# Optimization experiments

Hardware: AMD Instinct MI355X
Metric: run time of the kernel (lower is better)

The kernel has to match this reference:

```python
import jax, jax.numpy as jnp
import numpy as np

BN_EPS = 1e-5
N_NODES, N_EDGES, D_IN, HID = 100000, 1600000, 64, 128


def _bn(x, g, b, m, v):
    # BatchNorm1d in eval mode: running stats
    return (x - m) * jax.lax.rsqrt(v + BN_EPS) * g + b


def _gin_agg(x, edge_index, eps):
    # PyG GINConv aggregation: out[dst] = (1+eps)*x[dst] + sum_{src->dst} x[src]
    src, dst = edge_index[0], edge_index[1]
    s = jax.ops.segment_sum(x[src], dst, num_segments=x.shape[0])
    return (1.0 + eps) * x + s


def setup_inputs() -> dict:
    key = jax.random.key(0)
    ks = jax.random.split(key, 24)
    sc = 0.05
    d = {
        'x': jax.random.normal(ks[0], (N_NODES, D_IN), dtype=jnp.float32),
        'edge_index': jax.random.randint(ks[1], (2, N_EDGES), 0, N_NODES, dtype=jnp.int64),
        'eps1': jnp.zeros((), jnp.float32),
        'W1a': jax.random.normal(ks[2], (D_IN, HID), jnp.float32) * sc,
        'b1a': jnp.zeros((HID,), jnp.float32),
        'W1b': jax.random.normal(ks[3], (HID, HID), jnp.float32) * sc,
        'b1b': jnp.zeros((HID,), jnp.float32),
        'g1': jnp.ones((HID,), jnp.float32), 'be1': jnp.zeros((HID,), jnp.float32),
        'm1': jnp.zeros((HID,), jnp.float32), 'v1': jnp.ones((HID,), jnp.float32),
        'eps2': jnp.zeros((), jnp.float32),
        'W2a': jax.random.normal(ks[4], (HID, HID), jnp.float32) * sc,
        'b2a': jnp.zeros((HID,), jnp.float32),
        'g2': jnp.ones((HID,), jnp.float32), 'be2': jnp.zeros((HID,), jnp.float32),
        'm2': jnp.zeros((HID,), jnp.float32), 'v2': jnp.ones((HID,), jnp.float32),
        'eps3': jnp.zeros((), jnp.float32),
        'W3a': jax.random.normal(ks[5], (HID, HID), jnp.float32) * sc,
        'b3a': jnp.zeros((HID,), jnp.float32),
        'W3b': jax.random.normal(ks[6], (HID, HID), jnp.float32) * sc,
        'b3b': jnp.zeros((HID,), jnp.float32),
        'g3': jnp.ones((HID,), jnp.float32), 'be3': jnp.zeros((HID,), jnp.float32),
        'm3': jnp.zeros((HID,), jnp.float32), 'v3': jnp.ones((HID,), jnp.float32),
        'Wl': jax.random.normal(ks[7], (HID, HID), jnp.float32) * sc,
        'bl': jnp.zeros((HID,), jnp.float32),
        'Wf': jax.random.normal(ks[8], (HID, 1), jnp.float32) * sc,
        'bf': jnp.zeros((1,), jnp.float32),
    }
    return d


def reference(x, edge_index, eps1, W1a, b1a, W1b, b1b, g1, be1, m1, v1,
              eps2, W2a, b2a, g2, be2, m2, v2,
              eps3, W3a, b3a, W3b, b3b, g3, be3, m3, v3,
              Wl, bl, Wf, bf):
    # GINConv 1: agg -> Linear(64,128) ReLU -> Linear(128,128) ReLU -> BN
    h = _gin_agg(x, edge_index, eps1)
    h = jax.nn.relu(h @ W1a + b1a)
    h = jax.nn.relu(h @ W1b + b1b)
    h = _bn(h, g1, be1, m1, v1)
    # GINConv 2: agg -> Linear ReLU -> BN
    h = _gin_agg(h, edge_index, eps2)
    h = jax.nn.relu(h @ W2a + b2a)
    h = _bn(h, g2, be2, m2, v2)
    # GINConv 3: agg -> Linear ReLU -> Linear ReLU -> BN
    h = _gin_agg(h, edge_index, eps3)
    h = jax.nn.relu(h @ W3a + b3a)
    h = jax.nn.relu(h @ W3b + b3b)
    h = _bn(h, g3, be3, m3, v3)
    # head: lin1 + ReLU (dropout identity in eval), fc, squeeze
    h = jax.nn.relu(h @ Wl + bl)
    out = (h @ Wf + bf).squeeze(-1)  # [N]
    return out
```

## Files before the change

### kernel.cpp

```cpp
#include <hip/hip_runtime.h>


constexpr int NN  = 100000;
constexpr int NE  = 1600000;
constexpr int DIN = 64;
constexpr int HID = 128;

constexpr int BSH   = 9;
constexpr int NBUCK = 196;
constexpr int NBLK  = 200;
constexpr int CHUNK = 8000;

typedef __attribute__((ext_vector_type(4))) float f32x4;
typedef __attribute__((ext_vector_type(8))) short bf16x8;
typedef __attribute__((ext_vector_type(8))) unsigned short u16x8;

__device__ __forceinline__ short f2bf(float f) {
    union { float f; unsigned u; } x; x.f = f;
    unsigned r = x.u + 0x7fffu + ((x.u >> 16) & 1u);
    return (short)(r >> 16);
}
__device__ __forceinline__ float bf2f(short s) {
    union { unsigned u; float f; } x; x.u = ((unsigned)(unsigned short)s) << 16;
    return x.f;
}

__global__ __launch_bounds__(256)
void bhist_kernel(const int* __restrict__ eidx, int* __restrict__ bcnt,
                  int* __restrict__ pbase) {
    __shared__ int lh[NBUCK];
    int b = blockIdx.x;
    for (int i = threadIdx.x; i < NBUCK; i += 256) lh[i] = 0;
    __syncthreads();
    int e0 = b * CHUNK;
    for (int i = threadIdx.x; i < CHUNK; i += 256)
        atomicAdd(&lh[eidx[NE + e0 + i] >> BSH], 1);
    __syncthreads();
    for (int i = threadIdx.x; i < NBUCK; i += 256)
        pbase[b * NBUCK + i] = atomicAdd(&bcnt[i], lh[i]);
}

__global__ void bscan_kernel(const int* __restrict__ bcnt, int* __restrict__ bbase,
                             int* __restrict__ offs) {
    __shared__ int lds[256];
    int t = threadIdx.x;
    int v = (t < NBUCK) ? bcnt[t] : 0;
    lds[t] = v; __syncthreads();
    #pragma unroll
    for (int o = 1; o < 256; o <<= 1) {
        int x = (t >= o) ? lds[t - o] : 0;
        __syncthreads();
        lds[t] += x;
        __syncthreads();
    }
    if (t < NBUCK) bbase[t] = lds[t] - v;
    if (t == 0) { bbase[NBUCK] = NE; offs[NN] = NE; }
}

__global__ __launch_bounds__(256)
void part_kernel(const int* __restrict__ eidx, const int* __restrict__ bbase,
                 const int* __restrict__ pbase, int2* __restrict__ tmp) {
    __shared__ int lh[NBUCK], lofs[NBUCK], lcnt[NBUCK], gb[NBUCK];
    __shared__ int sb[256];
    __shared__ int2 lp[CHUNK];
    int b = blockIdx.x;
    int t = threadIdx.x;
    for (int i = t; i < NBUCK; i += 256) { lh[i] = 0; lcnt[i] = 0; }
    __syncthreads();
    int e0 = b * CHUNK;
    for (int i = t; i < CHUNK; i += 256)
        atomicAdd(&lh[eidx[NE + e0 + i] >> BSH], 1);
    __syncthreads();
    {
        int v = (t < NBUCK) ? lh[t] : 0;
        sb[t] = v; __syncthreads();
        #pragma unroll
        for (int o = 1; o < 256; o <<= 1) {
            int x = (t >= o) ? sb[t - o] : 0;
            __syncthreads();
            sb[t] += x;
            __syncthreads();
        }
        if (t < NBUCK) {
            lofs[t] = sb[t] - v;
            gb[t]   = bbase[t] + pbase[b * NBUCK + t];
        }
    }
    __syncthreads();
    for (int i = t; i < CHUNK; i += 256) {
        int s = eidx[e0 + i], d = eidx[NE + e0 + i];
        int bk = d >> BSH;
        int r = atomicAdd(&lcnt[bk], 1);
        lp[lofs[bk] + r] = int2{s, d};
    }
    __syncthreads();
    for (int i = t; i < CHUNK; i += 256) {
        int2 p = lp[i];
        int bk = p.y >> BSH;
        tmp[gb[bk] + (i - lofs[bk])] = p;
    }
}

__global__ __launch_bounds__(512)
void bsort_kernel(const int* __restrict__ bbase, const int2* __restrict__ tmp,
                  int* __restrict__ offs, int* __restrict__ esrc) {
    __shared__ int h[512], lo[512], cnt[512];
    int bk = blockIdx.x;
    int n0 = bk << BSH;
    int lo0 = bbase[bk], hi0 = bbase[bk + 1];
    int t = threadIdx.x;
    h[t] = 0; cnt[t] = 0;
    __syncthreads();
    for (int i = lo0 + t; i < hi0; i += 512)
        atomicAdd(&h[tmp[i].y - n0], 1);
    __syncthreads();
    int v = h[t];
    lo[t] = v; __syncthreads();
    #pragma unroll
    for (int o = 1; o < 512; o <<= 1) {
        int x = (t >= o) ? lo[t - o] : 0;
        __syncthreads();
        lo[t] += x;
        __syncthreads();
    }
    int excl = lo[t] - v;
    __syncthreads();
    lo[t] = excl;
    __syncthreads();
    if (n0 + t < NN) offs[n0 + t] = lo0 + excl;
    for (int i = lo0 + t; i < hi0; i += 512) {
        int2 p = tmp[i];
        int ld = p.y - n0;
        int r = atomicAdd(&cnt[ld], 1);
        esrc[lo0 + lo[ld] + r] = p.x;
    }
}

__global__ void cvt_kernel(const float* __restrict__ x, unsigned short* __restrict__ xb) {
    int i = blockIdx.x * 256 + threadIdx.x;
    if (i >= NN * DIN / 8) return;
    const f32x4* p = (const f32x4*)x + (size_t)i * 2;
    f32x4 v0 = p[0], v1 = p[1];
    u16x8 o;
    #pragma unroll
    for (int j = 0; j < 4; ++j) {
        o[j]     = (unsigned short)f2bf(v0[j]);
        o[j + 4] = (unsigned short)f2bf(v1[j]);
    }
    ((u16x8*)xb)[i] = o;
}

template<int D>
__global__ __launch_bounds__(256)
void aggb_kernel(const float* __restrict__ hf, const unsigned short* __restrict__ hb,
                 const int* __restrict__ offs, const int* __restrict__ esrc,
                 const float* __restrict__ epsp, float* __restrict__ out) {
    constexpr int TPN = D / 8;
    int node = blockIdx.x * (256 / TPN) + threadIdx.x / TPN;
    int f    = threadIdx.x % TPN;
    if (node >= NN) return;
    const u16x8* h8 = (const u16x8*)hb;
    float eps = 1.0f + *epsp;

    const float* hrow = hf + (size_t)node * D + f * 8;
    f32x4 a0 = *(const f32x4*)hrow * eps;
    f32x4 a1 = *(const f32x4*)(hrow + 4) * eps;
    f32x4 b0 = (f32x4)0.f, b1 = (f32x4)0.f;

    union { unsigned u; float fv; } cvt;
    auto acc8 = [&](u16x8 t, f32x4& x0, f32x4& x1) {
        #pragma unroll
        for (int j = 0; j < 4; ++j) { cvt.u = ((unsigned)t[j]) << 16;     x0[j] += cvt.fv; }
        #pragma unroll
        for (int j = 0; j < 4; ++j) { cvt.u = ((unsigned)t[j + 4]) << 16; x1[j] += cvt.fv; }
    };

    int k = offs[node], k1 = offs[node + 1];
    for (; k + 8 <= k1; k += 8) {
        int s0 = esrc[k+0], s1 = esrc[k+1], s2 = esrc[k+2], s3 = esrc[k+3];
        int s4 = esrc[k+4], s5 = esrc[k+5], s6 = esrc[k+6], s7 = esrc[k+7];
        u16x8 t0 = h8[(size_t)s0*TPN+f], t1 = h8[(size_t)s1*TPN+f];
        u16x8 t2 = h8[(size_t)s2*TPN+f], t3 = h8[(size_t)s3*TPN+f];
        u16x8 t4 = h8[(size_t)s4*TPN+f], t5 = h8[(size_t)s5*TPN+f];
        u16x8 t6 = h8[(size_t)s6*TPN+f], t7 = h8[(size_t)s7*TPN+f];
        acc8(t0, a0, a1); acc8(t1, b0, b1); acc8(t2, a0, a1); acc8(t3, b0, b1);
        acc8(t4, a0, a1); acc8(t5, b0, b1); acc8(t6, a0, a1); acc8(t7, b0, b1);
    }
    for (; k + 2 <= k1; k += 2) {
        u16x8 t0 = h8[(size_t)esrc[k]*TPN+f];
        u16x8 t1 = h8[(size_t)esrc[k+1]*TPN+f];
        acc8(t0, a0, a1); acc8(t1, b0, b1);
    }
    if (k < k1) acc8(h8[(size_t)esrc[k]*TPN+f], a0, a1);

    float* orow = out + (size_t)node * D + f * 8;
    *(f32x4*)orow       = a0 + b0;
    *(f32x4*)(orow + 4) = a1 + b1;
}

__global__ void packall_kernel(const float* __restrict__ W1a, const float* __restrict__ W1b,
                               const float* __restrict__ W2a, const float* __restrict__ W3a,
                               const float* __restrict__ W3b, const float* __restrict__ Wl,
                               short* P1a, short* P1b, short* P2a,
                               short* P3a, short* P3b, short* Pl) {
    const float* W; short* P; int K;
    switch (blockIdx.y) {
        case 0: W = W1a; P = P1a; K = 64;  break;
        case 1: W = W1b; P = P1b; K = 128; break;
        case 2: W = W2a; P = P2a; K = 128; break;
        case 3: W = W3a; P = P3a; K = 128; break;
        case 4: W = W3b; P = P3b; K = 128; break;
        default: W = Wl; P = Pl;  K = 128; break;
    }
    int T = (K / 32) * 8 * 64;
    int idx = blockIdx.x * 256 + threadIdx.x;
    if (idx >= T) return;
    int c  = idx >> 9;
    int nt = (idx >> 6) & 7;
    int l  = idx & 63;
    int col   = nt * 16 + (l & 15);
    int kbase = c * 32 + (l >> 4) * 8;
    bf16x8 hi, lo;
    #pragma unroll
    for (int j = 0; j < 8; ++j) {
        float w = W[(kbase + j) * HID + col];
        short h = f2bf(w);
        hi[j] = h;
        lo[j] = f2bf(w - bf2f(h));
    }
    *(bf16x8*)&P[(size_t)idx * 8]       = hi;
    *(bf16x8*)&P[(size_t)(T + idx) * 8] = lo;
}

__global__ __launch_bounds__(512)
void gemm_bn_kernel(const float* __restrict__ A, const short* __restrict__ P,
                    const float* __restrict__ bias,
                    const float* __restrict__ g, const float* __restrict__ be,
                    const float* __restrict__ m, const float* __restrict__ v,
                    float* __restrict__ out, unsigned short* __restrict__ hbout, int M) {
    constexpr int NCH = 4;
    constexpr int T   = NCH * 8 * 64;
    __shared__ short wlds[2 * T * 8];

    const int tid  = threadIdx.x;
    const int wid  = tid >> 6;
    const int lane = tid & 63;

    for (int i = tid; i < 2 * T; i += 512)
        ((bf16x8*)wlds)[i] = ((const bf16x8*)P)[i];
    __syncthreads();

    const int rlo  = lane & 15;
    const int kgrp = lane >> 4;
    const int row  = blockIdx.x * 128 + wid * 16 + rlo;
    const int r    = row < M ? row : M - 1;
    const float* arow = A + (size_t)r * 128 + kgrp * 8;

    f32x4 acc[8];
    #pragma unroll
    for (int i = 0; i < 8; ++i) acc[i] = (f32x4)0.0f;

    #pragma unroll
    for (int c = 0; c < NCH; ++c) {
        f32x4 a0 = *(const f32x4*)(arow + c * 32);
        f32x4 a1 = *(const f32x4*)(arow + c * 32 + 4);
        bf16x8 ah, al;
        #pragma unroll
        for (int j = 0; j < 4; ++j) {
            short h0 = f2bf(a0[j]);
            short h1 = f2bf(a1[j]);
            ah[j]     = h0;
            ah[j + 4] = h1;
            al[j]     = f2bf(a0[j] - bf2f(h0));
            al[j + 4] = f2bf(a1[j] - bf2f(h1));
        }
        #pragma unroll
        for (int nt = 0; nt < 8; ++nt) {
            int fi = ((c * 8) + nt) * 64 + lane;
            bf16x8 wh = *(bf16x8*)&wlds[(size_t)fi * 8];
            bf16x8 wl = *(bf16x8*)&wlds[(size_t)(T + fi) * 8];
            acc[nt] = __builtin_amdgcn_mfma_f32_16x16x32_bf16(ah, wh, acc[nt], 0, 0, 0);
            acc[nt] = __builtin_amdgcn_mfma_f32_16x16x32_bf16(al, wh, acc[nt], 0, 0, 0);
            acc[nt] = __builtin_amdgcn_mfma_f32_16x16x32_bf16(ah, wl, acc[nt], 0, 0, 0);
        }
    }

    #pragma unroll
    for (int nt = 0; nt < 8; ++nt) {
        int col  = nt * 16 + rlo;
        float bb = bias[col];
        float sv = g[col] * rsqrtf(v[col] + 1e-5f);
        float tv = be[col] - m[col] * sv;
        #pragma unroll
        for (int jj = 0; jj < 4; ++jj) {
            int rr = blockIdx.x * 128 + wid * 16 + kgrp * 4 + jj;
            float val = fmaxf(acc[nt][jj] + bb, 0.f) * sv + tv;
            if (rr < M) {
                out[(size_t)rr * 128 + col] = val;
                hbout[(size_t)rr * 128 + col] = (unsigned short)f2bf(val);
            }
        }
    }
}

template<int K1>
__global__ __launch_bounds__(256)
void fused2_kernel(const float* __restrict__ A,
                   const short* __restrict__ P1, const float* __restrict__ bias1,
                   const short* __restrict__ P2, const float* __restrict__ bias2,
                   const float* __restrict__ g, const float* __restrict__ be,
                   const float* __restrict__ m, const float* __restrict__ v,
                   float* __restrict__ out, unsigned short* __restrict__ hbout, int M) {
    constexpr int NCH1 = K1 / 32;
    constexpr int T1   = NCH1 * 8 * 64;
    constexpr int T2   = 4 * 8 * 64;
    constexpr int LDW  = 136;
    __shared__ short h1hi[64 * LDW];
    __shared__ short h1lo[64 * LDW];

    const int tid  = threadIdx.x;
    const int wid  = tid >> 6;
    const int lane = tid & 63;
    const int rlo  = lane & 15;
    const int kgrp = lane >> 4;

    const int row = blockIdx.x * 64 + wid * 16 + rlo;
    const int r   = row < M ? row : M - 1;
    const float* arow = A + (size_t)r * K1 + kgrp * 8;

    const bf16x8* P1v = (const bf16x8*)P1;
    const bf16x8* P2v = (const bf16x8*)P2;

    f32x4 acc[8];
    #pragma unroll
    for (int i = 0; i < 8; ++i) acc[i] = (f32x4)0.0f;

    #pragma unroll
    for (int c = 0; c < NCH1; ++c) {
        f32x4 a0 = *(const f32x4*)(arow + c * 32);
        f32x4 a1 = *(const f32x4*)(arow + c * 32 + 4);
        bf16x8 ah, al;
        #pragma unroll
        for (int j = 0; j < 4; ++j) {
            short h0 = f2bf(a0[j]);
            short h1 = f2bf(a1[j]);
            ah[j]     = h0;
            ah[j + 4] = h1;
            al[j]     = f2bf(a0[j] - bf2f(h0));
            al[j + 4] = f2bf(a1[j] - bf2f(h1));
        }
        #pragma unroll
        for (int nt = 0; nt < 8; ++nt) {
            int fi = ((c * 8) + nt) * 64 + lane;
            bf16x8 wh = P1v[fi];
            bf16x8 wl = P1v[T1 + fi];
            acc[nt] = __builtin_amdgcn_mfma_f32_16x16x32_bf16(ah, wh, acc[nt], 0, 0, 0);
            acc[nt] = __builtin_amdgcn_mfma_f32_16x16x32_bf16(al, wh, acc[nt], 0, 0, 0);
            acc[nt] = __builtin_amdgcn_mfma_f32_16x16x32_bf16(ah, wl, acc[nt], 0, 0, 0);
        }
    }

    #pragma unroll
    for (int nt = 0; nt < 8; ++nt) {
        int col  = nt * 16 + rlo;
        float bb = bias1[col];
        #pragma unroll
        for (int jj = 0; jj < 4; ++jj) {
            int lr = wid * 16 + kgrp * 4 + jj;
            float val = fmaxf(acc[nt][jj] + bb, 0.f);
            short h = f2bf(val);
            h1hi[lr * LDW + col] = h;
            h1lo[lr * LDW + col] = f2bf(val - bf2f(h));
        }
    }
    __syncthreads();

    f32x4 acc2[8];
    #pragma unroll
    for (int i = 0; i < 8; ++i) acc2[i] = (f32x4)0.0f;
    const int lr2 = wid * 16 + rlo;
    #pragma unroll
    for (int c = 0; c < 4; ++c) {
        bf16x8 ah = *(bf16x8*)&h1hi[lr2 * LDW + c * 32 + kgrp * 8];
        bf16x8 al = *(bf16x8*)&h1lo[lr2 * LDW + c * 32 + kgrp * 8];
        #pragma unroll
        for (int nt = 0; nt < 8; ++nt) {
            int fi = ((c * 8) + nt) * 64 + lane;
            bf16x8 wh = P2v[fi];
            bf16x8 wl = P2v[T2 + fi];
            acc2[nt] = __builtin_amdgcn_mfma_f32_16x16x32_bf16(ah, wh, acc2[nt], 0, 0, 0);
            acc2[nt] = __builtin_amdgcn_mfma_f32_16x16x32_bf16(al, wh, acc2[nt], 0, 0, 0);
            acc2[nt] = __builtin_amdgcn_mfma_f32_16x16x32_bf16(ah, wl, acc2[nt], 0, 0, 0);
        }
    }

    #pragma unroll
    for (int nt = 0; nt < 8; ++nt) {
        int col  = nt * 16 + rlo;
        float bb = bias2[col];
        float sv = g[col] * rsqrtf(v[col] + 1e-5f);
        float tv = be[col] - m[col] * sv;
        #pragma unroll
        for (int jj = 0; jj < 4; ++jj) {
            int rr = blockIdx.x * 64 + wid * 16 + kgrp * 4 + jj;
            float val = fmaxf(acc2[nt][jj] + bb, 0.f) * sv + tv;
            if (rr < M) {
                out[(size_t)rr * 128 + col] = val;
                hbout[(size_t)rr * 128 + col] = (unsigned short)f2bf(val);
            }
        }
    }
}

__global__ __launch_bounds__(256)
void fused3_kernel(const float* __restrict__ A,
                   const short* __restrict__ P1, const float* __restrict__ bias1,
                   const short* __restrict__ P2, const float* __restrict__ bias2,
                   const float* __restrict__ g, const float* __restrict__ be,
                   const float* __restrict__ m, const float* __restrict__ v,
                   const short* __restrict__ Pl, const float* __restrict__ bl,
                   const float* __restrict__ Wf, const float* __restrict__ bf,
                   float* __restrict__ out, int M) {
    constexpr int T  = 4 * 8 * 64;
    constexpr int LDW = 136;
    __shared__ short h1hi[64 * LDW];
    __shared__ short h1lo[64 * LDW];

    const int tid  = threadIdx.x;
    const int wid  = tid >> 6;
    const int lane = tid & 63;
    const int rlo  = lane & 15;
    const int kgrp = lane >> 4;

    const int row = blockIdx.x * 64 + wid * 16 + rlo;
    const int r   = row < M ? row : M - 1;
    const float* arow = A + (size_t)r * 128 + kgrp * 8;

    const bf16x8* P1v = (const bf16x8*)P1;
    const bf16x8* P2v = (const bf16x8*)P2;
    const bf16x8* Plv = (const bf16x8*)Pl;

    f32x4 acc[8];
    #pragma unroll
    for (int i = 0; i < 8; ++i) acc[i] = (f32x4)0.0f;
    #pragma unroll
    for (int c = 0; c < 4; ++c) {
        f32x4 a0 = *(const f32x4*)(arow + c * 32);
        f32x4 a1 = *(const f32x4*)(arow + c * 32 + 4);
        bf16x8 ah, al;
        #pragma unroll
        for (int j = 0; j < 4; ++j) {
            short h0 = f2bf(a0[j]);
            short h1 = f2bf(a1[j]);
            ah[j]     = h0;
            ah[j + 4] = h1;
            al[j]     = f2bf(a0[j] - bf2f(h0));
            al[j + 4] = f2bf(a1[j] - bf2f(h1));
        }
        #pragma unroll
        for (int nt = 0; nt < 8; ++nt) {
            int fi = ((c * 8) + nt) * 64 + lane;
            bf16x8 wh = P1v[fi];
            bf16x8 wl = P1v[T + fi];
            acc[nt] = __builtin_amdgcn_mfma_f32_16x16x32_bf16(ah, wh, acc[nt], 0, 0, 0);
            acc[nt] = __builtin_amdgcn_mfma_f32_16x16x32_bf16(al, wh, acc[nt], 0, 0, 0);
            acc[nt] = __builtin_amdgcn_mfma_f32_16x16x32_bf16(ah, wl, acc[nt], 0, 0, 0);
        }
    }
    #pragma unroll
    for (int nt = 0; nt < 8; ++nt) {
        int col  = nt * 16 + rlo;
        float bb = bias1[col];
        #pragma unroll
        for (int jj = 0; jj < 4; ++jj) {
            int lr = wid * 16 + kgrp * 4 + jj;
            float val = fmaxf(acc[nt][jj] + bb, 0.f);
            short h = f2bf(val);
            h1hi[lr * LDW + col] = h;
            h1lo[lr * LDW + col] = f2bf(val - bf2f(h));
        }
    }
    __syncthreads();

    const int lr2 = wid * 16 + rlo;
    bf16x8 ah2[4], al2[4];
    #pragma unroll
    for (int c = 0; c < 4; ++c) {
        ah2[c] = *(bf16x8*)&h1hi[lr2 * LDW + c * 32 + kgrp * 8];
        al2[c] = *(bf16x8*)&h1lo[lr2 * LDW + c * 32 + kgrp * 8];
    }
    __syncthreads();
    f32x4 acc2[8];
    #pragma unroll
    for (int i = 0; i < 8; ++i) acc2[i] = (f32x4)0.0f;
    #pragma unroll
    for (int c = 0; c < 4; ++c) {
        #pragma unroll
        for (int nt = 0; nt < 8; ++nt) {
            int fi = ((c * 8) + nt) * 64 + lane;
            bf16x8 wh = P2v[fi];
            bf16x8 wl = P2v[T + fi];
            acc2[nt] = __builtin_amdgcn_mfma_f32_16x16x32_bf16(ah2[c], wh, acc2[nt], 0, 0, 0);
            acc2[nt] = __builtin_amdgcn_mfma_f32_16x16x32_bf16(al2[c], wh, acc2[nt], 0, 0, 0);
            acc2[nt] = __builtin_amdgcn_mfma_f32_16x16x32_bf16(ah2[c], wl, acc2[nt], 0, 0, 0);
        }
    }
    #pragma unroll
    for (int nt = 0; nt < 8; ++nt) {
        int col  = nt * 16 + rlo;
        float bb = bias2[col];
        float sv = g[col] * rsqrtf(v[col] + 1e-5f);
        float tv = be[col] - m[col] * sv;
        #pragma unroll
        for (int jj = 0; jj < 4; ++jj) {
            int lr = wid * 16 + kgrp * 4 + jj;
            float val = fmaxf(acc2[nt][jj] + bb, 0.f) * sv + tv;
            short h = f2bf(val);
            h1hi[lr * LDW + col] = h;
            h1lo[lr * LDW + col] = f2bf(val - bf2f(h));
        }
    }
    __syncthreads();

    bf16x8 ah3[4], al3[4];
    #pragma unroll
    for (int c = 0; c < 4; ++c) {
        ah3[c] = *(bf16x8*)&h1hi[lr2 * LDW + c * 32 + kgrp * 8];
        al3[c] = *(bf16x8*)&h1lo[lr2 * LDW + c * 32 + kgrp * 8];
    }
    f32x4 acc3[8];
    #pragma unroll
    for (int i = 0; i < 8; ++i) acc3[i] = (f32x4)0.0f;
    #pragma unroll
    for (int c = 0; c < 4; ++c) {
        #pragma unroll
        for (int nt = 0; nt < 8; ++nt) {
            int fi = ((c * 8) + nt) * 64 + lane;
            bf16x8 wh = Plv[fi];
            bf16x8 wl = Plv[T + fi];
            acc3[nt] = __builtin_amdgcn_mfma_f32_16x16x32_bf16(ah3[c], wh, acc3[nt], 0, 0, 0);
            acc3[nt] = __builtin_amdgcn_mfma_f32_16x16x32_bf16(al3[c], wh, acc3[nt], 0, 0, 0);
            acc3[nt] = __builtin_amdgcn_mfma_f32_16x16x32_bf16(ah3[c], wl, acc3[nt], 0, 0, 0);
        }
    }
    float p0 = 0, p1 = 0, p2 = 0, p3 = 0;
    #pragma unroll
    for (int nt = 0; nt < 8; ++nt) {
        int col  = nt * 16 + rlo;
        float bb = bl[col];
        float wv = Wf[col];
        p0 += fmaxf(acc3[nt][0] + bb, 0.f) * wv;
        p1 += fmaxf(acc3[nt][1] + bb, 0.f) * wv;
        p2 += fmaxf(acc3[nt][2] + bb, 0.f) * wv;
        p3 += fmaxf(acc3[nt][3] + bb, 0.f) * wv;
    }
    #pragma unroll
    for (int o = 1; o < 16; o <<= 1) {
        p0 += __shfl_xor(p0, o);
        p1 += __shfl_xor(p1, o);
        p2 += __shfl_xor(p2, o);
        p3 += __shfl_xor(p3, o);
    }
    if (rlo == 0) {
        int rbase = blockIdx.x * 64 + wid * 16 + kgrp * 4;
        float bfv = bf[0];
        if (rbase + 0 < M) out[rbase + 0] = p0 + bfv;
        if (rbase + 1 < M) out[rbase + 1] = p1 + bfv;
        if (rbase + 2 < M) out[rbase + 2] = p2 + bfv;
        if (rbase + 3 < M) out[rbase + 3] = p3 + bfv;
    }
}

extern "C" void kernel_launch(void* const* d_in, const int* in_sizes, int n_in,
                              void* d_out, int out_size, void* d_ws, size_t ws_size,
                              hipStream_t stream) {
    const float* x    = (const float*)d_in[0];
    const int*   eidx = (const int*)d_in[1];
    const float* eps1 = (const float*)d_in[2];
    const float* W1a  = (const float*)d_in[3];
    const float* b1a  = (const float*)d_in[4];
    const float* W1b  = (const float*)d_in[5];
    const float* b1b  = (const float*)d_in[6];
    const float* g1   = (const float*)d_in[7];
    const float* be1  = (const float*)d_in[8];
    const float* m1   = (const float*)d_in[9];
    const float* v1   = (const float*)d_in[10];
    const float* eps2 = (const float*)d_in[11];
    const float* W2a  = (const float*)d_in[12];
    const float* b2a  = (const float*)d_in[13];
    const float* g2   = (const float*)d_in[14];
    const float* be2  = (const float*)d_in[15];
    const float* m2   = (const float*)d_in[16];
    const float* v2   = (const float*)d_in[17];
    const float* eps3 = (const float*)d_in[18];
    const float* W3a  = (const float*)d_in[19];
    const float* b3a  = (const float*)d_in[20];
    const float* W3b  = (const float*)d_in[21];
    const float* b3b  = (const float*)d_in[22];
    const float* g3   = (const float*)d_in[23];
    const float* be3  = (const float*)d_in[24];
    const float* m3   = (const float*)d_in[25];
    const float* v3   = (const float*)d_in[26];
    const float* Wl   = (const float*)d_in[27];
    const float* bl   = (const float*)d_in[28];
    const float* Wf   = (const float*)d_in[29];
    const float* bfp  = (const float*)d_in[30];

    char* ws = (char*)d_ws;
    size_t off = 0;
    auto alloc = [&](size_t bytes) -> void* {
        off = (off + 255) & ~(size_t)255;
        void* p = ws + off;
        off += bytes;
        return p;
    };

    float*          bufA = (float*)alloc((size_t)NN * 128 * 4);
    float*          bufB = (float*)alloc((size_t)NN * 128 * 4);
    unsigned short* hb   = (unsigned short*)alloc((size_t)NN * 128 * 2);
    int*   offs   = (int*)alloc((size_t)(NN + 1) * 4);
    int*   esrc   = (int*)alloc((size_t)NE * 4);
    int*   bcnt   = (int*)alloc((size_t)NBUCK * 4);
    int*   bbase  = (int*)alloc((size_t)(NBUCK + 1) * 4);
    int*   pbase  = (int*)alloc((size_t)NBLK * NBUCK * 4);
    short* P1a    = (short*)alloc((size_t)2 * DIN * HID * 2);
    short* P1b    = (short*)alloc((size_t)2 * HID * HID * 2);
    short* P2a    = (short*)alloc((size_t)2 * HID * HID * 2);
    short* P3a    = (short*)alloc((size_t)2 * HID * HID * 2);
    short* P3b    = (short*)alloc((size_t)2 * HID * HID * 2);
    short* Pl     = (short*)alloc((size_t)2 * HID * HID * 2);
    int2*  tmp    = (int2*)bufA;

    const int GRID_G    = (NN + 127) / 128;
    const int GRID_F    = (NN + 63) / 64;
    const int GRID_A64  = (NN + 31) / 32;
    const int GRID_A128 = (NN + 15) / 16;

    hipMemsetAsync(bcnt, 0, (size_t)NBUCK * 4, stream);
    bhist_kernel<<<NBLK, 256, 0, stream>>>(eidx, bcnt, pbase);
    bscan_kernel<<<1, 256, 0, stream>>>(bcnt, bbase, offs);
    part_kernel<<<NBLK, 256, 0, stream>>>(eidx, bbase, pbase, tmp);
    bsort_kernel<<<NBUCK, 512, 0, stream>>>(bbase, tmp, offs, esrc);

    {
        dim3 grid(8, 6);
        packall_kernel<<<grid, 256, 0, stream>>>(W1a, W1b, W2a, W3a, W3b, Wl,
                                                 P1a, P1b, P2a, P3a, P3b, Pl);
    }
    cvt_kernel<<<(NN * DIN / 8 + 255) / 256, 256, 0, stream>>>(x, hb);

    aggb_kernel<64><<<GRID_A64, 256, 0, stream>>>(x, hb, offs, esrc, eps1, bufA);
    fused2_kernel<64><<<GRID_F, 256, 0, stream>>>(bufA, P1a, b1a, P1b, b1b,
                                                  g1, be1, m1, v1, bufB, hb, NN);
    aggb_kernel<128><<<GRID_A128, 256, 0, stream>>>(bufB, hb, offs, esrc, eps2, bufA);
    gemm_bn_kernel<<<GRID_G, 512, 0, stream>>>(bufA, P2a, b2a, g2, be2, m2, v2,
                                               bufB, hb, NN);
    aggb_kernel<128><<<GRID_A128, 256, 0, stream>>>(bufB, hb, offs, esrc, eps3, bufA);
    fused3_kernel<<<GRID_F, 256, 0, stream>>>(bufA, P3a, b3a, P3b, b3b,
                                              g3, be3, m3, v3, Pl, bl, Wf, bfp,
                                              (float*)d_out, NN);
}
```

Baseline: 388.3 us.

## Process two row tiles per wave in fused MLP kernels, drop block barriers

The fused2 and fused3 kernels now run 128-thread blocks in which each wave handles two 16-row tiles (rows r and r+32). Each loaded weight fragment is reused for twice as many MFMAs. Because every wave now reads back only the LDS rows it wrote itself, the __syncthreads calls are replaced by a wave-local lgkmcnt wait fence. This should halve weight fragment loads per row and remove block-level synchronisation, at the cost of twice as many accumulator registers, which may lower occupancy or cause spills.

```diff
diff --git a/kernel.cpp b/kernel.cpp
--- a/kernel.cpp
+++ b/kernel.cpp
@@ -23,6 +23,12 @@
 __device__ __forceinline__ float bf2f(short s) {
     union { unsigned u; float f; } x; x.u = ((unsigned)(unsigned short)s) << 16;
     return x.f;
+}
+
+__device__ __forceinline__ void wave_lds_fence() {
+    __builtin_amdgcn_sched_barrier(0);
+    asm volatile("s_waitcnt lgkmcnt(0)" ::: "memory");
+    __builtin_amdgcn_sched_barrier(0);
 }
 
 __global__ __launch_bounds__(256)
@@ -304,7 +310,7 @@
 }
 
 template<int K1>
-__global__ __launch_bounds__(256)
+__global__ __launch_bounds__(128)
 void fused2_kernel(const float* __restrict__ A,
                    const short* __restrict__ P1, const float* __restrict__ bias1,
                    const short* __restrict__ P2, const float* __restrict__ bias2,
@@ -324,39 +330,46 @@
     const int rlo  = lane & 15;
     const int kgrp = lane >> 4;
 
-    const int row = blockIdx.x * 64 + wid * 16 + rlo;
-    const int r   = row < M ? row : M - 1;
-    const float* arow = A + (size_t)r * K1 + kgrp * 8;
+    const int rowA = blockIdx.x * 64 + wid * 16 + rlo;
+    const int rowB = rowA + 32;
+    const int rA   = rowA < M ? rowA : M - 1;
+    const int rB   = rowB < M ? rowB : M - 1;
+    const float* arowA = A + (size_t)rA * K1 + kgrp * 8;
+    const float* arowB = A + (size_t)rB * K1 + kgrp * 8;
 
     const bf16x8* P1v = (const bf16x8*)P1;
     const bf16x8* P2v = (const bf16x8*)P2;
 
-    f32x4 acc[8];
-    #pragma unroll
-    for (int i = 0; i < 8; ++i) acc[i] = (f32x4)0.0f;
+    f32x4 accA[8], accB[8];
+    #pragma unroll
+    for (int i = 0; i < 8; ++i) { accA[i] = (f32x4)0.0f; accB[i] = (f32x4)0.0f; }
 
     #pragma unroll
     for (int c = 0; c < NCH1; ++c) {
-        f32x4 a0 = *(const f32x4*)(arow + c * 32);
-        f32x4 a1 = *(const f32x4*)(arow + c * 32 + 4);
-        bf16x8 ah, al;
+        f32x4 aA0 = *(const f32x4*)(arowA + c * 32);
+        f32x4 aA1 = *(const f32x4*)(arowA + c * 32 + 4);
+        f32x4 aB0 = *(const f32x4*)(arowB + c * 32);
+        f32x4 aB1 = *(const f32x4*)(arowB + c * 32 + 4);
+        bf16x8 ahA, alA, ahB, alB;
         #pragma unroll
         for (int j = 0; j < 4; ++j) {
-            short h0 = f2bf(a0[j]);
-            short h1 = f2bf(a1[j]);
-            ah[j]     = h0;
-            ah[j + 4] = h1;
-            al[j]     = f2bf(a0[j] - bf2f(h0));
-            al[j + 4] = f2bf(a1[j] - bf2f(h1));
+            short h;
+            h = f2bf(aA0[j]); ahA[j]   = h; alA[j]   = f2bf(aA0[j] - bf2f(h));
+            h = f2bf(aA1[j]); ahA[j+4] = h; alA[j+4] = f2bf(aA1[j] - bf2f(h));
+            h = f2bf(aB0[j]); ahB[j]   = h; alB[j]   = f2bf(aB0[j] - bf2f(h));
+            h = f2bf(aB1[j]); ahB[j+4] = h; alB[j+4] = f2bf(aB1[j] - bf2f(h));
         }
         #pragma unroll
         for (int nt = 0; nt < 8; ++nt) {
             int fi = ((c * 8) + nt) * 64 + lane;
             bf16x8 wh = P1v[fi];
             bf16x8 wl = P1v[T1 + fi];
-            acc[nt] = __builtin_amdgcn_mfma_f32_16x16x32_bf16(ah, wh, acc[nt], 0, 0, 0);
-            acc[nt] = __builtin_amdgcn_mfma_f32_16x16x32_bf16(al, wh, acc[nt], 0, 0, 0);
-            acc[nt] = __builtin_amdgcn_mfma_f32_16x16x32_bf16(ah, wl, acc[nt], 0, 0, 0);
+            accA[nt] = __builtin_amdgcn_mfma_f32_16x16x32_bf16(ahA, wh, accA[nt], 0, 0, 0);
+            accA[nt] = __builtin_amdgcn_mfma_f32_16x16x32_bf16(alA, wh, accA[nt], 0, 0, 0);
+            accA[nt] = __builtin_amdgcn_mfma_f32_16x16x32_bf16(ahA, wl, accA[nt], 0, 0, 0);
+            accB[nt] = __builtin_amdgcn_mfma_f32_16x16x32_bf16(ahB, wh, accB[nt], 0, 0, 0);
+            accB[nt] = __builtin_amdgcn_mfma_f32_16x16x32_bf16(alB, wh, accB[nt], 0, 0, 0);
+            accB[nt] = __builtin_amdgcn_mfma_f32_16x16x32_bf16(ahB, wl, accB[nt], 0, 0, 0);
         }
     }
 
@@ -366,31 +379,41 @@
         float bb = bias1[col];
         #pragma unroll
         for (int jj = 0; jj < 4; ++jj) {
-            int lr = wid * 16 + kgrp * 4 + jj;
-            float val = fmaxf(acc[nt][jj] + bb, 0.f);
-            short h = f2bf(val);
-            h1hi[lr * LDW + col] = h;
-            h1lo[lr * LDW + col] = f2bf(val - bf2f(h));
-        }
-    }
-    __syncthreads();
-
-    f32x4 acc2[8];
-    #pragma unroll
-    for (int i = 0; i < 8; ++i) acc2[i] = (f32x4)0.0f;
-    const int lr2 = wid * 16 + rlo;
+            int lrA = wid * 16 + kgrp * 4 + jj;
+            float vA = fmaxf(accA[nt][jj] + bb, 0.f);
+            short hA = f2bf(vA);
+            h1hi[lrA * LDW + col] = hA;
+            h1lo[lrA * LDW + col] = f2bf(vA - bf2f(hA));
+            int lrB = lrA + 32;
+            float vB = fmaxf(accB[nt][jj] + bb, 0.f);
+            short hB = f2bf(vB);
+            h1hi[lrB * LDW + col] = hB;
+            h1lo[lrB * LDW + col] = f2bf(vB - bf2f(hB));
+        }
+    }
+    wave_lds_fence();
+
+    #pragma unroll
+    for (int i = 0; i < 8; ++i) { accA[i] = (f32x4)0.0f; accB[i] = (f32x4)0.0f; }
+    const int lrA2 = wid * 16 + rlo;
+    const int lrB2 = lrA2 + 32;
     #pragma unroll
     for (int c = 0; c < 4; ++c) {
-        bf16x8 ah = *(bf16x8*)&h1hi[lr2 * LDW + c * 32 + kgrp * 8];
-        bf16x8 al = *(bf16x8*)&h1lo[lr2 * LDW + c * 32 + kgrp * 8];
+        bf16x8 ahA = *(bf16x8*)&h1hi[lrA2 * LDW + c * 32 + kgrp * 8];
+        bf16x8 alA = *(bf16x8*)&h1lo[lrA2 * LDW + c * 32 + kgrp * 8];
+        bf16x8 ahB = *(bf16x8*)&h1hi[lrB2 * LDW + c * 32 + kgrp * 8];
+        bf16x8 alB = *(bf16x8*)&h1lo[lrB2 * LDW + c * 32 + kgrp * 8];
         #pragma unroll
         for (int nt = 0; nt < 8; ++nt) {
             int fi = ((c * 8) + nt) * 64 + lane;
             bf16x8 wh = P2v[fi];
             bf16x8 wl = P2v[T2 + fi];
-            acc2[nt] = __builtin_amdgcn_mfma_f32_16x16x32_bf16(ah, wh, acc2[nt], 0, 0, 0);
-            acc2[nt] = __builtin_amdgcn_mfma_f32_16x16x32_bf16(al, wh, acc2[nt], 0, 0, 0);
-            acc2[nt] = __builtin_amdgcn_mfma_f32_16x16x32_bf16(ah, wl, acc2[nt], 0, 0, 0);
+            accA[nt] = __builtin_amdgcn_mfma_f32_16x16x32_bf16(ahA, wh, accA[nt], 0, 0, 0);
+            accA[nt] = __builtin_amdgcn_mfma_f32_16x16x32_bf16(alA, wh, accA[nt], 0, 0, 0);
+            accA[nt] = __builtin_amdgcn_mfma_f32_16x16x32_bf16(ahA, wl, accA[nt], 0, 0, 0);
+            accB[nt] = __builtin_amdgcn_mfma_f32_16x16x32_bf16(ahB, wh, accB[nt], 0, 0, 0);
+            accB[nt] = __builtin_amdgcn_mfma_f32_16x16x32_bf16(alB, wh, accB[nt], 0, 0, 0);
+            accB[nt] = __builtin_amdgcn_mfma_f32_16x16x32_bf16(ahB, wl, accB[nt], 0, 0, 0);
         }
     }
 
@@ -402,17 +425,23 @@
         float tv = be[col] - m[col] * sv;
         #pragma unroll
         for (int jj = 0; jj < 4; ++jj) {
-            int rr = blockIdx.x * 64 + wid * 16 + kgrp * 4 + jj;
-            float val = fmaxf(acc2[nt][jj] + bb, 0.f) * sv + tv;
-            if (rr < M) {
-                out[(size_t)rr * 128 + col] = val;
-                hbout[(size_t)rr * 128 + col] = (unsigned short)f2bf(val);
+            int rrA = blockIdx.x * 64 + wid * 16 + kgrp * 4 + jj;
+            float vA = fmaxf(accA[nt][jj] + bb, 0.f) * sv + tv;
+            if (rrA < M) {
+                out[(size_t)rrA * 128 + col] = vA;
+                hbout[(size_t)rrA * 128 + col] = (unsigned short)f2bf(vA);
             }
-        }
-    }
-}
-
-__global__ __launch_bounds__(256)
+            int rrB = rrA + 32;
+            float vB = fmaxf(accB[nt][jj] + bb, 0.f) * sv + tv;
+            if (rrB < M) {
+                out[(size_t)rrB * 128 + col] = vB;
+                hbout[(size_t)rrB * 128 + col] = (unsigned short)f2bf(vB);
+            }
+        }
+    }
+}
+
+__global__ __launch_bounds__(128)
 void fused3_kernel(const float* __restrict__ A,
                    const short* __restrict__ P1, const float* __restrict__ bias1,
                    const short* __restrict__ P2, const float* __restrict__ bias2,
@@ -432,39 +461,47 @@
     const int rlo  = lane & 15;
     const int kgrp = lane >> 4;
 
-    const int row = blockIdx.x * 64 + wid * 16 + rlo;
-    const int r   = row < M ? row : M - 1;
-    const float* arow = A + (size_t)r * 128 + kgrp * 8;
+    const int rowA = blockIdx.x * 64 + wid * 16 + rlo;
+    const int rowB = rowA + 32;
+    const int rA   = rowA < M ? rowA : M - 1;
+    const int rB   = rowB < M ? rowB : M - 1;
+    const float* arowA = A + (size_t)rA * 128 + kgrp * 8;
+    const float* arowB = A + (size_t)rB * 128 + kgrp * 8;
 
     const bf16x8* P1v = (const bf16x8*)P1;
     const bf16x8* P2v = (const bf16x8*)P2;
     const bf16x8* Plv = (const bf16x8*)Pl;
 
-    f32x4 acc[8];
-    #pragma unroll
-    for (int i = 0; i < 8; ++i) acc[i] = (f32x4)0.0f;
+    f32x4 accA[8], accB[8];
+    #pragma unroll
+    for (int i = 0; i < 8; ++i) { accA[i] = (f32x4)0.0f; accB[i] = (f32x4)0.0f; }
+
     #pragma unroll
     for (int c = 0; c < 4; ++c) {
-        f32x4 a0 = *(const f32x4*)(arow + c * 32);
-        f32x4 a1 = *(const f32x4*)(arow + c * 32 + 4);
-        bf16x8 ah, al;
+        f32x4 aA0 = *(const f32x4*)(arowA + c * 32);
+        f32x4 aA1 = *(const f32x4*)(arowA + c * 32 + 4);
+        f32x4 aB0 = *(const f32x4*)(arowB + c * 32);
+        f32x4 aB1 = *(const f32x4*)(arowB + c * 32 + 4);
+        bf16x8 ahA, alA, ahB, alB;
         #pragma unroll
         for (int j = 0; j < 4; ++j) {
-            short h0 = f2bf(a0[j]);
-            short h1 = f2bf(a1[j]);
-            ah[j]     = h0;
-            ah[j + 4] = h1;
-            al[j]     = f2bf(a0[j] - bf2f(h0));
-            al[j + 4] = f2bf(a1[j] - bf2f(h1));
+            short h;
+            h = f2bf(aA0[j]); ahA[j]   = h; alA[j]   = f2bf(aA0[j] - bf2f(h));
+            h = f2bf(aA1[j]); ahA[j+4] = h; alA[j+4] = f2bf(aA1[j] - bf2f(h));
+            h = f2bf(aB0[j]); ahB[j]   = h; alB[j]   = f2bf(aB0[j] - bf2f(h));
+            h = f2bf(aB1[j]); ahB[j+4] = h; alB[j+4] = f2bf(aB1[j] - bf2f(h));
         }
         #pragma unroll
         for (int nt = 0; nt < 8; ++nt) {
             int fi = ((c * 8) + nt) * 64 + lane;
             bf16x8 wh = P1v[fi];
             bf16x8 wl = P1v[T + fi];
-            acc[nt] = __builtin_amdgcn_mfma_f32_16x16x32_bf16(ah, wh, acc[nt], 0, 0, 0);
-            acc[nt] = __builtin_amdgcn_mfma_f32_16x16x32_bf16(al, wh, acc[nt], 0, 0, 0);
-            acc[nt] = __builtin_amdgcn_mfma_f32_16x16x32_bf16(ah, wl, acc[nt], 0, 0, 0);
+            accA[nt] = __builtin_amdgcn_mfma_f32_16x16x32_bf16(ahA, wh, accA[nt], 0, 0, 0);
+            accA[nt] = __builtin_amdgcn_mfma_f32_16x16x32_bf16(alA, wh, accA[nt], 0, 0, 0);
+            accA[nt] = __builtin_amdgcn_mfma_f32_16x16x32_bf16(ahA, wl, accA[nt], 0, 0, 0);
+            accB[nt] = __builtin_amdgcn_mfma_f32_16x16x32_bf16(ahB, wh, accB[nt], 0, 0, 0);
+            accB[nt] = __builtin_amdgcn_mfma_f32_16x16x32_bf16(alB, wh, accB[nt], 0, 0, 0);
+            accB[nt] = __builtin_amdgcn_mfma_f32_16x16x32_bf16(ahB, wl, accB[nt], 0, 0, 0);
         }
     }
     #pragma unroll
@@ -473,38 +510,44 @@
         float bb = bias1[col];
         #pragma unroll
         for (int jj = 0; jj < 4; ++jj) {
-            int lr = wid * 16 + kgrp * 4 + jj;
-            float val = fmaxf(acc[nt][jj] + bb, 0.f);
-            short h = f2bf(val);
-            h1hi[lr * LDW + col] = h;
-            h1lo[lr * LDW + col] = f2bf(val - bf2f(h));
-        }
-    }
-    __syncthreads();
-
-    const int lr2 = wid * 16 + rlo;
-    bf16x8 ah2[4], al2[4];
+            int lrA = wid * 16 + kgrp * 4 + jj;
+            float vA = fmaxf(accA[nt][jj] + bb, 0.f);
+            short hA = f2bf(vA);
+            h1hi[lrA * LDW + col] = hA;
+            h1lo[lrA * LDW + col] = f2bf(vA - bf2f(hA));
+            int lrB = lrA + 32;
+            float vB = fmaxf(accB[nt][jj] + bb, 0.f);
+            short hB = f2bf(vB);
+            h1hi[lrB * LDW + col] = hB;
+            h1lo[lrB * LDW + col] = f2bf(vB - bf2f(hB));
+        }
+    }
+    wave_lds_fence();
+
+    const int lrA2 = wid * 16 + rlo;
+    const int lrB2 = lrA2 + 32;
+    #pragma unroll
+    for (int i = 0; i < 8; ++i) { accA[i] = (f32x4)0.0f; accB[i] = (f32x4)0.0f; }
     #pragma unroll
     for (int c = 0; c < 4; ++c) {
-        ah2[c] = *(bf16x8*)&h1hi[lr2 * LDW + c * 32 + kgrp * 8];
-        al2[c] = *(bf16x8*)&h1lo[lr2 * LDW + c * 32 + kgrp * 8];
-    }
-    __syncthreads();
-    f32x4 acc2[8];
-    #pragma unroll
-    for (int i = 0; i < 8; ++i) acc2[i] = (f32x4)0.0f;
-    #pragma unroll
-    for (int c = 0; c < 4; ++c) {
+        bf16x8 ahA = *(bf16x8*)&h1hi[lrA2 * LDW + c * 32 + kgrp * 8];
+        bf16x8 alA = *(bf16x8*)&h1lo[lrA2 * LDW + c * 32 + kgrp * 8];
+        bf16x8 ahB = *(bf16x8*)&h1hi[lrB2 * LDW + c * 32 + kgrp * 8];
+        bf16x8 alB = *(bf16x8*)&h1lo[lrB2 * LDW + c * 32 + kgrp * 8];
         #pragma unroll
         for (int nt = 0; nt < 8; ++nt) {
             int fi = ((c * 8) + nt) * 64 + lane;
             bf16x8 wh = P2v[fi];
             bf16x8 wl = P2v[T + fi];
-            acc2[nt] = __builtin_amdgcn_mfma_f32_16x16x32_bf16(ah2[c], wh, acc2[nt], 0, 0, 0);
-            acc2[nt] = __builtin_amdgcn_mfma_f32_16x16x32_bf16(al2[c], wh, acc2[nt], 0, 0, 0);
-            acc2[nt] = __builtin_amdgcn_mfma_f32_16x16x32_bf16(ah2[c], wl, acc2[nt], 0, 0, 0);
-        }
-    }
+            accA[nt] = __builtin_amdgcn_mfma_f32_16x16x32_bf16(ahA, wh, accA[nt], 0, 0, 0);
+            accA[nt] = __builtin_amdgcn_mfma_f32_16x16x32_bf16(alA, wh, accA[nt], 0, 0, 0);
+            accA[nt] = __builtin_amdgcn_mfma_f32_16x16x32_bf16(ahA, wl, accA[nt], 0, 0, 0);
+            accB[nt] = __builtin_amdgcn_mfma_f32_16x16x32_bf16(ahB, wh, accB[nt], 0, 0, 0);
+            accB[nt] = __builtin_amdgcn_mfma_f32_16x16x32_bf16(alB, wh, accB[nt], 0, 0, 0);
+            accB[nt] = __builtin_amdgcn_mfma_f32_16x16x32_bf16(ahB, wl, accB[nt], 0, 0, 0);
+        }
+    }
+    wave_lds_fence();
     #pragma unroll
     for (int nt = 0; nt < 8; ++nt) {
         int col  = nt * 16 + rlo;
@@ -513,61 +556,76 @@
         float tv = be[col] - m[col] * sv;
         #pragma unroll
         for (int jj = 0; jj < 4; ++jj) {
-            int lr = wid * 16 + kgrp * 4 + jj;
-            float val = fmaxf(acc2[nt][jj] + bb, 0.f) * sv + tv;
-            short h = f2bf(val);
-            h1hi[lr * LDW + col] = h;
-            h1lo[lr * LDW + col] = f2bf(val - bf2f(h));
-        }
-    }
-    __syncthreads();
-
-    bf16x8 ah3[4], al3[4];
+            int lrA = wid * 16 + kgrp * 4 + jj;
+            float vA = fmaxf(accA[nt][jj] + bb, 0.f) * sv + tv;
+            short hA = f2bf(vA);
+            h1hi[lrA * LDW + col] = hA;
+            h1lo[lrA * LDW + col] = f2bf(vA - bf2f(hA));
+            int lrB = lrA + 32;
+            float vB = fmaxf(accB[nt][jj] + bb, 0.f) * sv + tv;
+            short hB = f2bf(vB);
+            h1hi[lrB * LDW + col] = hB;
+            h1lo[lrB * LDW + col] = f2bf(vB - bf2f(hB));
+        }
+    }
+    wave_lds_fence();
+
+    #pragma unroll
+    for (int i = 0; i < 8; ++i) { accA[i] = (f32x4)0.0f; accB[i] = (f32x4)0.0f; }
     #pragma unroll
     for (int c = 0; c < 4; ++c) {
-        ah3[c] = *(bf16x8*)&h1hi[lr2 * LDW + c * 32 + kgrp * 8];
-        al3[c] = *(bf16x8*)&h1lo[lr2 * LDW + c * 32 + kgrp * 8];
-    }
-    f32x4 acc3[8];
-    #pragma unroll
-    for (int i = 0; i < 8; ++i) acc3[i] = (f32x4)0.0f;
-    #pragma unroll
-    for (int c = 0; c < 4; ++c) {
+        bf16x8 ahA = *(bf16x8*)&h1hi[lrA2 * LDW + c * 32 + kgrp * 8];
+        bf16x8 alA = *(bf16x8*)&h1lo[lrA2 * LDW + c * 32 + kgrp * 8];
+        bf16x8 ahB = *(bf16x8*)&h1hi[lrB2 * LDW + c * 32 + kgrp * 8];
+        bf16x8 alB = *(bf16x8*)&h1lo[lrB2 * LDW + c * 32 + kgrp * 8];
         #pragma unroll
         for (int nt = 0; nt < 8; ++nt) {
             int fi = ((c * 8) + nt) * 64 + lane;
             bf16x8 wh = Plv[fi];
             bf16x8 wl = Plv[T + fi];
-            acc3[nt] = __builtin_amdgcn_mfma_f32_16x16x32_bf16(ah3[c], wh, acc3[nt], 0, 0, 0);
-            acc3[nt] = __builtin_amdgcn_mfma_f32_16x16x32_bf16(al3[c], wh, acc3[nt], 0, 0, 0);
-            acc3[nt] = __builtin_amdgcn_mfma_f32_16x16x32_bf16(ah3[c], wl, acc3[nt], 0, 0, 0);
-        }
-    }
-    float p0 = 0, p1 = 0, p2 = 0, p3 = 0;
+            accA[nt] = __builtin_amdgcn_mfma_f32_16x16x32_bf16(ahA, wh, accA[nt], 0, 0, 0);
+            accA[nt] = __builtin_amdgcn_mfma_f32_16x16x32_bf16(alA, wh, accA[nt], 0, 0, 0);
+            accA[nt] = __builtin_amdgcn_mfma_f32_16x16x32_bf16(ahA, wl, accA[nt], 0, 0, 0);
+            accB[nt] = __builtin_amdgcn_mfma_f32_16x16x32_bf16(ahB, wh, accB[nt], 0, 0, 0);
+            accB[nt] = __builtin_amdgcn_mfma_f32_16x16x32_bf16(alB, wh, accB[nt], 0, 0, 0);
+            accB[nt] = __builtin_amdgcn_mfma_f32_16x16x32_bf16(ahB, wl, accB[nt], 0, 0, 0);
+        }
+    }
+    float pA0 = 0, pA1 = 0, pA2 = 0, pA3 = 0;
+    float pB0 = 0, pB1 = 0, pB2 = 0, pB3 = 0;
     #pragma unroll
     for (int nt = 0; nt < 8; ++nt) {
         int col  = nt * 16 + rlo;
         float bb = bl[col];
         float wv = Wf[col];
-        p0 += fmaxf(acc3[nt][0] + bb, 0.f) * wv;
-        p1 += fmaxf(acc3[nt][1] + bb, 0.f) * wv;
-        p2 += fmaxf(acc3[nt][2] + bb, 0.f) * wv;
-        p3 += fmaxf(acc3[nt][3] + bb, 0.f) * wv;
+        pA0 += fmaxf(accA[nt][0] + bb, 0.f) * wv;
+        pA1 += fmaxf(accA[nt][1] + bb, 0.f) * wv;
+        pA2 += fmaxf(accA[nt][2] + bb, 0.f) * wv;
+        pA3 += fmaxf(accA[nt][3] + bb, 0.f) * wv;
+        pB0 += fmaxf(accB[nt][0] + bb, 0.f) * wv;
+        pB1 += fmaxf(accB[nt][1] + bb, 0.f) * wv;
+        pB2 += fmaxf(accB[nt][2] + bb, 0.f) * wv;
+        pB3 += fmaxf(accB[nt][3] + bb, 0.f) * wv;
     }
     #pragma unroll
     for (int o = 1; o < 16; o <<= 1) {
-        p0 += __shfl_xor(p0, o);
-        p1 += __shfl_xor(p1, o);
-        p2 += __shfl_xor(p2, o);
-        p3 += __shfl_xor(p3, o);
+        pA0 += __shfl_xor(pA0, o); pA1 += __shfl_xor(pA1, o);
+        pA2 += __shfl_xor(pA2, o); pA3 += __shfl_xor(pA3, o);
+        pB0 += __shfl_xor(pB0, o); pB1 += __shfl_xor(pB1, o);
+        pB2 += __shfl_xor(pB2, o); pB3 += __shfl_xor(pB3, o);
     }
     if (rlo == 0) {
         int rbase = blockIdx.x * 64 + wid * 16 + kgrp * 4;
         float bfv = bf[0];
-        if (rbase + 0 < M) out[rbase + 0] = p0 + bfv;
-        if (rbase + 1 < M) out[rbase + 1] = p1 + bfv;
-        if (rbase + 2 < M) out[rbase + 2] = p2 + bfv;
-        if (rbase + 3 < M) out[rbase + 3] = p3 + bfv;
+        if (rbase + 0 < M) out[rbase + 0] = pA0 + bfv;
+        if (rbase + 1 < M) out[rbase + 1] = pA1 + bfv;
+        if (rbase + 2 < M) out[rbase + 2] = pA2 + bfv;
+        if (rbase + 3 < M) out[rbase + 3] = pA3 + bfv;
+        int rb2 = rbase + 32;
+        if (rb2 + 0 < M) out[rb2 + 0] = pB0 + bfv;
+        if (rb2 + 1 < M) out[rb2 + 1] = pB1 + bfv;
+        if (rb2 + 2 < M) out[rb2 + 2] = pB2 + bfv;
+        if (rb2 + 3 < M) out[rb2 + 3] = pB3 + bfv;
     }
 }
 
@@ -650,13 +708,13 @@
     cvt_kernel<<<(NN * DIN / 8 + 255) / 256, 256, 0, stream>>>(x, hb);
 
     aggb_kernel<64><<<GRID_A64, 256, 0, stream>>>(x, hb, offs, esrc, eps1, bufA);
-    fused2_kernel<64><<<GRID_F, 256, 0, stream>>>(bufA, P1a, b1a, P1b, b1b,
+    fused2_kernel<64><<<GRID_F, 128, 0, stream>>>(bufA, P1a, b1a, P1b, b1b,
                                                   g1, be1, m1, v1, bufB, hb, NN);
     aggb_kernel<128><<<GRID_A128, 256, 0, stream>>>(bufB, hb, offs, esrc, eps2, bufA);
     gemm_bn_kernel<<<GRID_G, 512, 0, stream>>>(bufA, P2a, b2a, g2, be2, m2, v2,
                                                bufB, hb, NN);
     aggb_kernel<128><<<GRID_A128, 256, 0, stream>>>(bufB, hb, offs, esrc, eps3, bufA);
-    fused3_kernel<<<GRID_F, 256, 0, stream>>>(bufA, P3a, b3a, P3b, b3b,
+    fused3_kernel<<<GRID_F, 128, 0, stream>>>(bufA, P3a, b3a, P3b, b3b,
                                               g3, be3, m3, v3, Pl, bl, Wf, bfp,
                                               (float*)d_out, NN);
 }
```

New measurement: 368.4 us. 5.1% less time.
